# Optimization experiments

Hardware: AMD Instinct MI355X
Metric: run time of the kernel (lower is better)

## Reference

```python
import jax, jax.numpy as jnp
import numpy as np

L = 2        # lags
D = 8        # latent_size
H = 64       # hidden_dim
IN = L * D + 1
SLOPE = 0.2  # nn.LeakyReLU(0.2) as in the LEAP/TDRL NLayerLeakyMLP


def setup_inputs() -> dict:
    key = jax.random.key(0)
    ks = jax.random.split(key, 6)
    B, T = 128, 514
    def w(k, shape, fan_in):
        return jax.random.normal(k, shape, jnp.float32) * (1.0 / np.sqrt(fan_in))
    return {
        'x':  jax.random.normal(ks[0], (B, T, D), jnp.float32),
        # per-latent-dim stacked MLP params (D independent small MLPs)
        'W0': w(ks[1], (D, H, IN), IN), 'b0': jnp.zeros((D, H), jnp.float32),
        'W1': w(ks[2], (D, H, H), H),   'b1': jnp.zeros((D, H), jnp.float32),
        'W2': w(ks[3], (D, H, H), H),   'b2': jnp.zeros((D, H), jnp.float32),
        'Wo': w(ks[4], (D, 1, H), H),   'bo': jnp.zeros((D, 1), jnp.float32),
    }


def reference(x, W0, b0, W1, b1, W2, b2, Wo, bo):
    B, T, Dd = x.shape
    W = T - L                                   # number of windows
    N = B * W
    idx = jnp.arange(W)[:, None] + jnp.arange(L + 1)[None, :]
    xw = x[:, idx]                              # [B, W, L+1, D]
    yy = xw[:, :, :L].reshape(N, L * Dd)        # lagged history  [N, L*D]
    xx = xw[:, :, L].reshape(N, Dd)             # current step    [N, D]
    # per-dim inputs: concat(yy, xx[:, i])  -> [D, N, IN]
    inp = jnp.concatenate(
        [jnp.broadcast_to(yy[None], (Dd, N, L * Dd)), xx.T[:, :, None]], axis=-1)

    def lin(a, Wm, bm):  # batched over latent dim d
        return jnp.einsum('dni,dhi->dnh', a, Wm) + bm[:, None, :]

    h0 = lin(inp, W0, b0); m0 = jnp.where(h0 > 0, 1.0, SLOPE); a0 = h0 * m0
    h1 = lin(a0, W1, b1);  m1 = jnp.where(h1 > 0, 1.0, SLOPE); a1 = h1 * m1
    h2 = lin(a1, W2, b2);  m2 = jnp.where(h2 > 0, 1.0, SLOPE); a2 = h2 * m2
    out = jnp.einsum('dnh,doh->dno', a2, Wo) + bo[:, None, :]   # [D, N, 1]

    # analytic Jacobian of scalar output wrt input: Wo diag(m2) W2 diag(m1) W1 diag(m0) W0
    g = jnp.broadcast_to(Wo[:, 0][:, None, :], (Dd, N, H)) * m2
    g = jnp.einsum('dnh,dhg->dng', g, W2) * m1
    g = jnp.einsum('dnh,dhg->dng', g, W1) * m0
    jac = jnp.einsum('dnh,dhi->dni', g, W0)                     # [D, N, IN]

    residuals = out[:, :, 0].T.reshape(B, W, Dd)                # [B, W, D]
    logabsdet = jnp.sum(jnp.log(jnp.abs(jac[:, :, -1])), axis=0)  # sum over dims -> [N]
    sum_log_abs_det_jacobian = logabsdet.reshape(B, W).sum(axis=1)  # [B]
    hist_jac = jac[:, :, :-1]                                   # [D, N, L*D] (stacked list)
    return residuals, sum_log_abs_det_jacobian, hist_jac
```

## Files before the change

### kernel.cpp

```cpp
#include <hip/hip_runtime.h>
#include <hip/hip_bf16.h>
#include <math.h>

#define D_ 8
#define H_ 64
#define IN_ 17
#define SLOPE_ 0.2f
#define B_ 128
#define T_ 514
#define W_ 512
#define N_ (B_*W_)
#define RES_SZ (N_*D_)
#define LOG_OFF RES_SZ
#define HJ_OFF (RES_SZ + B_)

#define BSTR 72

#define PERD_B 23040
#define OB_W2H 0
#define OB_W2L 4608
#define OB_W1H 9216
#define OB_W1L 13824
#define OB_W0H 18432
#define OB_W0L 20736
#define FWD_U (D_*PERD_B)
#define PERD_F 27648
#define OF_W0H 0
#define OF_W0L 4608
#define OF_W1H 9216
#define OF_W1L 13824
#define OF_W2H 18432
#define OF_W2L 23040

typedef __attribute__((ext_vector_type(8))) short short8;
typedef __attribute__((ext_vector_type(4))) float float4v;

__device__ __forceinline__ unsigned short f2bf(float x) {
    return __bfloat16_as_ushort(__float2bfloat16(x));
}
__device__ __forceinline__ float bf2f(unsigned short h) {
    return __uint_as_float(((unsigned)h) << 16);
}
__device__ __forceinline__ void split2(float x, short& hi, short& lo) {
    unsigned short h = f2bf(x);
    hi = (short)h;
    float r = x - bf2f(h);
    lo = (short)f2bf(r);
}

__global__ void setup_kernel(const float* __restrict__ W0, const float* __restrict__ W1,
                             const float* __restrict__ W2,
                             unsigned short* __restrict__ ws, float* __restrict__ out) {
    int d = blockIdx.x;
    unsigned short* bb = ws + d * PERD_B;
    unsigned short* bf = ws + FWD_U + d * PERD_F;
    for (int idx = threadIdx.x; idx < H_ * H_; idx += blockDim.x) {
        int r = idx >> 6, c = idx & 63;
        float v2 = W2[d * H_ * H_ + c * H_ + r];
        unsigned short h2 = f2bf(v2);
        bb[OB_W2H + r * BSTR + c] = h2;
        bb[OB_W2L + r * BSTR + c] = f2bf(v2 - bf2f(h2));
        float v1 = W1[d * H_ * H_ + c * H_ + r];
        unsigned short h1 = f2bf(v1);
        bb[OB_W1H + r * BSTR + c] = h1;
        bb[OB_W1L + r * BSTR + c] = f2bf(v1 - bf2f(h1));
        float f1v = W1[(d * H_ + r) * H_ + c];
        unsigned short f1h = f2bf(f1v);
        bf[OF_W1H + r * BSTR + c] = f1h;
        bf[OF_W1L + r * BSTR + c] = f2bf(f1v - bf2f(f1h));
        float f2v = W2[(d * H_ + r) * H_ + c];
        unsigned short f2h = f2bf(f2v);
        bf[OF_W2H + r * BSTR + c] = f2h;
        bf[OF_W2L + r * BSTR + c] = f2bf(f2v - bf2f(f2h));
    }
    for (int idx = threadIdx.x; idx < 32 * H_; idx += blockDim.x) {
        int nn = idx >> 6, k = idx & 63;
        float v = (nn < IN_) ? W0[(d * H_ + k) * IN_ + nn] : 0.0f;
        unsigned short h = f2bf(v);
        bb[OB_W0H + nn * BSTR + k] = h;
        bb[OB_W0L + nn * BSTR + k] = f2bf(v - bf2f(h));
        float fv = (nn < IN_) ? W0[(d * H_ + k) * IN_ + nn] : 0.0f;
        unsigned short fh = f2bf(fv);
        bf[OF_W0H + k * BSTR + nn] = fh;
        bf[OF_W0L + k * BSTR + nn] = f2bf(fv - bf2f(fh));
    }
    if (d == 0 && threadIdx.x < B_) out[LOG_OFF + threadIdx.x] = 0.0f;
}

__global__ __launch_bounds__(256, 2) void fwdm_kernel(
    const float* __restrict__ x,
    const float* __restrict__ b0, const float* __restrict__ b1,
    const float* __restrict__ b2, const float* __restrict__ Wo,
    const float* __restrict__ bo, const unsigned short* __restrict__ ws,
    float* __restrict__ out)
{
    __shared__ __align__(16) unsigned short sB[PERD_F];
    __shared__ __align__(16) float sAct[4 * 16 * 68];
    __shared__ unsigned sM0[256*2], sM1[256*2], sM2[256*2];
    __shared__ __align__(16) float sWo[H_];

    const int blk = blockIdx.x;
    const int d   = blk >> 8;
    const int t   = blk & 255;
    const int tid = threadIdx.x;
    const int n0  = t << 8;

    {
        const uint4* src = (const uint4*)(ws + FWD_U + d * PERD_F);
        uint4* dst = (uint4*)sB;
        for (int i = tid; i < PERD_F / 8; i += 256) dst[i] = src[i];
        if (tid < H_) sWo[tid] = Wo[d * H_ + tid];
    }

    const int wv   = tid >> 6;
    const int lane = tid & 63;
    const int q    = lane >> 4;
    const int c    = lane & 15;
    float* slot = sAct + wv * (16 * 68);

    float b0v[4], b1v[4], b2v[4];
#pragma unroll
    for (int nt = 0; nt < 4; ++nt) {
        b0v[nt] = b0[d * H_ + nt * 16 + c];
        b1v[nt] = b1[d * H_ + nt * 16 + c];
        b2v[nt] = b2[d * H_ + nt * 16 + c];
    }
    const float bod = bo[d];
    __syncthreads();

#pragma unroll 1
    for (int mti = 0; mti < 4; ++mti) {
        const int sbase = wv * 64 + mti * 16;
        const int gn    = n0 + sbase + c;

        short8 ah[2], al[2];
        float4v acc[4];

        {
            const float* xp = x + (((gn >> 9) * T_) + (gn & 511)) * D_;
            float xs[8] = {0,0,0,0,0,0,0,0};
            if (q < 2) {
                float4 f0 = *(const float4*)(xp + q * 8);
                float4 f1 = *(const float4*)(xp + q * 8 + 4);
                xs[0]=f0.x; xs[1]=f0.y; xs[2]=f0.z; xs[3]=f0.w;
                xs[4]=f1.x; xs[5]=f1.y; xs[6]=f1.z; xs[7]=f1.w;
            } else if (q == 2) {
                xs[0] = xp[16 + d];
            }
#pragma unroll
            for (int j = 0; j < 8; ++j) { short h8,l8; split2(xs[j],h8,l8); ah[0][j]=h8; al[0][j]=l8; }
        }
#pragma unroll
        for (int nt = 0; nt < 4; ++nt) {
            int off = (nt*16 + c) * BSTR + (q << 3);
            short8 bh = *(const short8*)(sB + OF_W0H + off);
            short8 bl = *(const short8*)(sB + OF_W0L + off);
            float4v a = {0.f,0.f,0.f,0.f};
            a = __builtin_amdgcn_mfma_f32_16x16x32_bf16(ah[0], bh, a, 0,0,0);
            a = __builtin_amdgcn_mfma_f32_16x16x32_bf16(al[0], bh, a, 0,0,0);
            a = __builtin_amdgcn_mfma_f32_16x16x32_bf16(ah[0], bl, a, 0,0,0);
            acc[nt] = a;
        }
#pragma unroll
        for (int r = 0; r < 4; ++r) {
            float hv[4]; bool p[4];
#pragma unroll
            for (int nt = 0; nt < 4; ++nt) { hv[nt] = acc[nt][r] + b0v[nt]; p[nt] = hv[nt] > 0.0f; }
            unsigned long long B0 = __ballot(p[0]), B1 = __ballot(p[1]);
            unsigned long long B2 = __ballot(p[2]), B3 = __ballot(p[3]);
            if (c == 0) {
                int row = sbase + q * 4 + r;
                sM0[row*2]   = (unsigned)((B0 >> (q*16)) & 0xffffull) | ((unsigned)((B1 >> (q*16)) & 0xffffull) << 16);
                sM0[row*2+1] = (unsigned)((B2 >> (q*16)) & 0xffffull) | ((unsigned)((B3 >> (q*16)) & 0xffffull) << 16);
            }
#pragma unroll
            for (int nt = 0; nt < 4; ++nt)
                slot[(q*4+r)*68 + nt*16 + c] = p[nt] ? hv[nt] : hv[nt] * SLOPE_;
        }

#pragma unroll
        for (int kst = 0; kst < 2; ++kst) {
            const float* p = slot + c * 68 + kst * 32 + q * 8;
            float4 f0 = *(const float4*)p, f1 = *(const float4*)(p + 4);
            float xs[8] = {f0.x,f0.y,f0.z,f0.w,f1.x,f1.y,f1.z,f1.w};
#pragma unroll
            for (int j = 0; j < 8; ++j) { short h8,l8; split2(xs[j],h8,l8); ah[kst][j]=h8; al[kst][j]=l8; }
        }
#pragma unroll
        for (int nt = 0; nt < 4; ++nt) {
            float4v a = {0.f,0.f,0.f,0.f};
#pragma unroll
            for (int kst = 0; kst < 2; ++kst) {
                int off = (nt*16 + c) * BSTR + (kst << 5) + (q << 3);
                short8 bh = *(const short8*)(sB + OF_W1H + off);
                short8 bl = *(const short8*)(sB + OF_W1L + off);
                a = __builtin_amdgcn_mfma_f32_16x16x32_bf16(ah[kst], bh, a, 0,0,0);
                a = __builtin_amdgcn_mfma_f32_16x16x32_bf16(al[kst], bh, a, 0,0,0);
                a = __builtin_amdgcn_mfma_f32_16x16x32_bf16(ah[kst], bl, a, 0,0,0);
            }
            acc[nt] = a;
        }
#pragma unroll
        for (int r = 0; r < 4; ++r) {
            float hv[4]; bool p[4];
#pragma unroll
            for (int nt = 0; nt < 4; ++nt) { hv[nt] = acc[nt][r] + b1v[nt]; p[nt] = hv[nt] > 0.0f; }
            unsigned long long B0 = __ballot(p[0]), B1 = __ballot(p[1]);
            unsigned long long B2 = __ballot(p[2]), B3 = __ballot(p[3]);
            if (c == 0) {
                int row = sbase + q * 4 + r;
                sM1[row*2]   = (unsigned)((B0 >> (q*16)) & 0xffffull) | ((unsigned)((B1 >> (q*16)) & 0xffffull) << 16);
                sM1[row*2+1] = (unsigned)((B2 >> (q*16)) & 0xffffull) | ((unsigned)((B3 >> (q*16)) & 0xffffull) << 16);
            }
#pragma unroll
            for (int nt = 0; nt < 4; ++nt)
                slot[(q*4+r)*68 + nt*16 + c] = p[nt] ? hv[nt] : hv[nt] * SLOPE_;
        }

#pragma unroll
        for (int kst = 0; kst < 2; ++kst) {
            const float* p = slot + c * 68 + kst * 32 + q * 8;
            float4 f0 = *(const float4*)p, f1 = *(const float4*)(p + 4);
            float xs[8] = {f0.x,f0.y,f0.z,f0.w,f1.x,f1.y,f1.z,f1.w};
#pragma unroll
            for (int j = 0; j < 8; ++j) { short h8,l8; split2(xs[j],h8,l8); ah[kst][j]=h8; al[kst][j]=l8; }
        }
#pragma unroll
        for (int nt = 0; nt < 4; ++nt) {
            float4v a = {0.f,0.f,0.f,0.f};
#pragma unroll
            for (int kst = 0; kst < 2; ++kst) {
                int off = (nt*16 + c) * BSTR + (kst << 5) + (q << 3);
                short8 bh = *(const short8*)(sB + OF_W2H + off);
                short8 bl = *(const short8*)(sB + OF_W2L + off);
                a = __builtin_amdgcn_mfma_f32_16x16x32_bf16(ah[kst], bh, a, 0,0,0);
                a = __builtin_amdgcn_mfma_f32_16x16x32_bf16(al[kst], bh, a, 0,0,0);
                a = __builtin_amdgcn_mfma_f32_16x16x32_bf16(ah[kst], bl, a, 0,0,0);
            }
            acc[nt] = a;
        }
#pragma unroll
        for (int r = 0; r < 4; ++r) {
            float hv[4]; bool p[4];
#pragma unroll
            for (int nt = 0; nt < 4; ++nt) { hv[nt] = acc[nt][r] + b2v[nt]; p[nt] = hv[nt] > 0.0f; }
            unsigned long long B0 = __ballot(p[0]), B1 = __ballot(p[1]);
            unsigned long long B2 = __ballot(p[2]), B3 = __ballot(p[3]);
            if (c == 0) {
                int row = sbase + q * 4 + r;
                sM2[row*2]   = (unsigned)((B0 >> (q*16)) & 0xffffull) | ((unsigned)((B1 >> (q*16)) & 0xffffull) << 16);
                sM2[row*2+1] = (unsigned)((B2 >> (q*16)) & 0xffffull) | ((unsigned)((B3 >> (q*16)) & 0xffffull) << 16);
            }
#pragma unroll
            for (int nt = 0; nt < 4; ++nt)
                slot[(q*4+r)*68 + nt*16 + c] = p[nt] ? hv[nt] : hv[nt] * SLOPE_;
        }

        {
            const float* srow = slot + c * 68 + q * 16;
            const float* wop  = sWo + q * 16;
            float4 s0 = *(const float4*)srow,       s1 = *(const float4*)(srow + 4);
            float4 s2 = *(const float4*)(srow + 8), s3 = *(const float4*)(srow + 12);
            float4 w0 = *(const float4*)wop,        w1 = *(const float4*)(wop + 4);
            float4 w2 = *(const float4*)(wop + 8),  w3 = *(const float4*)(wop + 12);
            float part = s0.x*w0.x + s0.y*w0.y + s0.z*w0.z + s0.w*w0.w
                       + s1.x*w1.x + s1.y*w1.y + s1.z*w1.z + s1.w*w1.w
                       + s2.x*w2.x + s2.y*w2.y + s2.z*w2.z + s2.w*w2.w
                       + s3.x*w3.x + s3.y*w3.y + s3.z*w3.z + s3.w*w3.w;
            part += __shfl_xor(part, 16, 64);
            part += __shfl_xor(part, 32, 64);
            if (q == 0) out[gn * D_ + d] = part + bod;
        }
    }

    __syncthreads();
    {
        unsigned* outU = (unsigned*)out;
        size_t mi = (size_t)HJ_OFF + ((size_t)d * N_ + (n0 + tid)) * 16;
        outU[mi+0] = sM0[tid*2]; outU[mi+1] = sM0[tid*2+1];
        outU[mi+2] = sM1[tid*2]; outU[mi+3] = sM1[tid*2+1];
        outU[mi+4] = sM2[tid*2]; outU[mi+5] = sM2[tid*2+1];
    }
}

__global__ __launch_bounds__(256, 2) void bwd_kernel(
    const float* __restrict__ Wo,
    const unsigned short* __restrict__ ws,
    float* __restrict__ out)
{
    __shared__ __align__(16) unsigned short sB[PERD_B];
    __shared__ __align__(16) float sAct[4 * 16 * 68];
    __shared__ unsigned sM0[256*2], sM1[256*2], sM2[256*2];
    __shared__ float sWo[H_];
    __shared__ float sRed[4];

    const int blk = blockIdx.x;
    const int d   = blk >> 8;
    const int t   = blk & 255;
    const int tid = threadIdx.x;
    const int n0  = t << 8;

    {
        const uint4* src = (const uint4*)(ws + d * PERD_B);
        uint4* dst = (uint4*)sB;
        for (int i = tid; i < PERD_B / 8; i += 256) dst[i] = src[i];
        if (tid < H_) sWo[tid] = Wo[d * H_ + tid];
        const unsigned* outU = (const unsigned*)out;
        size_t mi = (size_t)HJ_OFF + ((size_t)d * N_ + (n0 + tid)) * 16;
        sM0[tid*2] = outU[mi+0]; sM0[tid*2+1] = outU[mi+1];
        sM1[tid*2] = outU[mi+2]; sM1[tid*2+1] = outU[mi+3];
        sM2[tid*2] = outU[mi+4]; sM2[tid*2+1] = outU[mi+5];
    }
    __syncthreads();

    const int wv   = tid >> 6;
    const int lane = tid & 63;
    const int q    = lane >> 4;
    const int c    = lane & 15;
    float* slot = sAct + wv * (16 * 68);

    short8 Bw2h[4][2], Bw2l[4][2], Bw1h[4][2], Bw1l[4][2], Bw0h[2][2], Bw0l[2][2];
#pragma unroll
    for (int nt = 0; nt < 4; ++nt)
#pragma unroll
        for (int kst = 0; kst < 2; ++kst) {
            int off = (nt*16 + c) * BSTR + (kst << 5) + (q << 3);
            Bw2h[nt][kst] = *(const short8*)(sB + OB_W2H + off);
            Bw2l[nt][kst] = *(const short8*)(sB + OB_W2L + off);
            Bw1h[nt][kst] = *(const short8*)(sB + OB_W1H + off);
            Bw1l[nt][kst] = *(const short8*)(sB + OB_W1L + off);
        }
#pragma unroll
    for (int nt = 0; nt < 2; ++nt)
#pragma unroll
        for (int kst = 0; kst < 2; ++kst) {
            int off = (nt*16 + c) * BSTR + (kst << 5) + (q << 3);
            Bw0h[nt][kst] = *(const short8*)(sB + OB_W0H + off);
            Bw0l[nt][kst] = *(const short8*)(sB + OB_W0L + off);
        }

    float ld = 0.0f;

#pragma unroll 1
    for (int mti = 0; mti < 4; ++mti) {
        const int sbase = wv * 64 + mti * 16;

        short8 ah[2];
        float4v acc[4];

#pragma unroll
        for (int kst = 0; kst < 2; ++kst) {
            unsigned mm = sM2[(sbase + c) * 2 + kst];
            const float* wop = sWo + kst * 32 + q * 8;
            float4 e0 = *(const float4*)wop, e1 = *(const float4*)(wop + 4);
            float xs[8] = {e0.x,e0.y,e0.z,e0.w,e1.x,e1.y,e1.z,e1.w};
#pragma unroll
            for (int j = 0; j < 8; ++j) {
                int kk = q * 8 + j;
                float v = xs[j] * (((mm >> kk) & 1u) ? 1.0f : SLOPE_);
                ah[kst][j] = (short)f2bf(v);
            }
        }
#pragma unroll
        for (int nt = 0; nt < 4; ++nt) {
            float4v a = {0.f,0.f,0.f,0.f};
#pragma unroll
            for (int kst = 0; kst < 2; ++kst) {
                a = __builtin_amdgcn_mfma_f32_16x16x32_bf16(ah[kst], Bw2h[nt][kst], a, 0,0,0);
                a = __builtin_amdgcn_mfma_f32_16x16x32_bf16(ah[kst], Bw2l[nt][kst], a, 0,0,0);
            }
            acc[nt] = a;
        }
#pragma unroll
        for (int nt = 0; nt < 4; ++nt)
#pragma unroll
            for (int r = 0; r < 4; ++r) {
                int row = q * 4 + r, col = nt * 16 + c;
                unsigned bit = (sM1[(sbase + row) * 2 + (col >> 5)] >> (col & 31)) & 1u;
                float v = acc[nt][r];
                slot[row * 68 + col] = bit ? v : v * SLOPE_;
            }

#pragma unroll
        for (int kst = 0; kst < 2; ++kst) {
            const float* p = slot + c * 68 + kst * 32 + q * 8;
            float4 f0 = *(const float4*)p, f1 = *(const float4*)(p + 4);
            float xs[8] = {f0.x,f0.y,f0.z,f0.w,f1.x,f1.y,f1.z,f1.w};
#pragma unroll
            for (int j = 0; j < 8; ++j) ah[kst][j] = (short)f2bf(xs[j]);
        }
#pragma unroll
        for (int nt = 0; nt < 4; ++nt) {
            float4v a = {0.f,0.f,0.f,0.f};
#pragma unroll
            for (int kst = 0; kst < 2; ++kst) {
                a = __builtin_amdgcn_mfma_f32_16x16x32_bf16(ah[kst], Bw1h[nt][kst], a, 0,0,0);
                a = __builtin_amdgcn_mfma_f32_16x16x32_bf16(ah[kst], Bw1l[nt][kst], a, 0,0,0);
            }
            acc[nt] = a;
        }
#pragma unroll
        for (int nt = 0; nt < 4; ++nt)
#pragma unroll
            for (int r = 0; r < 4; ++r) {
                int row = q * 4 + r, col = nt * 16 + c;
                unsigned bit = (sM0[(sbase + row) * 2 + (col >> 5)] >> (col & 31)) & 1u;
                float v = acc[nt][r];
                slot[row * 68 + col] = bit ? v : v * SLOPE_;
            }

#pragma unroll
        for (int kst = 0; kst < 2; ++kst) {
            const float* p = slot + c * 68 + kst * 32 + q * 8;
            float4 f0 = *(const float4*)p, f1 = *(const float4*)(p + 4);
            float xs[8] = {f0.x,f0.y,f0.z,f0.w,f1.x,f1.y,f1.z,f1.w};
#pragma unroll
            for (int j = 0; j < 8; ++j) ah[kst][j] = (short)f2bf(xs[j]);
        }
#pragma unroll
        for (int nt = 0; nt < 2; ++nt) {
            float4v a = {0.f,0.f,0.f,0.f};
#pragma unroll
            for (int kst = 0; kst < 2; ++kst) {
                a = __builtin_amdgcn_mfma_f32_16x16x32_bf16(ah[kst], Bw0h[nt][kst], a, 0,0,0);
                a = __builtin_amdgcn_mfma_f32_16x16x32_bf16(ah[kst], Bw0l[nt][kst], a, 0,0,0);
            }
            acc[nt] = a;
        }
#pragma unroll
        for (int r = 0; r < 4; ++r) {
            int gn = n0 + sbase + q * 4 + r;
            out[HJ_OFF + ((size_t)d * N_ + gn) * 16 + c] = acc[0][r];
        }
        if (c == 0) {
#pragma unroll
            for (int r = 0; r < 4; ++r) ld += logf(fabsf(acc[1][r]));
        }
    }

#pragma unroll
    for (int off = 32; off > 0; off >>= 1)
        ld += __shfl_down(ld, off, 64);
    if (lane == 0) sRed[wv] = ld;
    __syncthreads();
    if (tid == 0)
        atomicAdd(out + LOG_OFF + (t >> 1), (sRed[0] + sRed[1]) + (sRed[2] + sRed[3]));
}

extern "C" void kernel_launch(void* const* d_in, const int* in_sizes, int n_in,
                              void* d_out, int out_size, void* d_ws, size_t ws_size,
                              hipStream_t stream) {
    const float* x  = (const float*)d_in[0];
    const float* W0 = (const float*)d_in[1];
    const float* b0 = (const float*)d_in[2];
    const float* W1 = (const float*)d_in[3];
    const float* b1 = (const float*)d_in[4];
    const float* W2 = (const float*)d_in[5];
    const float* b2 = (const float*)d_in[6];
    const float* Wo = (const float*)d_in[7];
    const float* bo = (const float*)d_in[8];
    float* out = (float*)d_out;
    unsigned short* ws = (unsigned short*)d_ws;

    hipLaunchKernelGGL(setup_kernel, dim3(D_), dim3(256), 0, stream, W0, W1, W2, ws, out);
    hipLaunchKernelGGL(fwdm_kernel, dim3(D_ * 256), dim3(256), 0, stream,
                       x, b0, b1, b2, Wo, bo, ws, out);
    hipLaunchKernelGGL(bwd_kernel, dim3(D_ * 256), dim3(256), 0, stream,
                       Wo, ws, out);
}
```

Measured before the change: 217.5 us.

## Fuse forward and backward Jacobian kernels into a single launch

Merges the forward (activation and mask) kernel and the backward Jacobian kernel into one kernel. The leaky-ReLU masks stay in shared memory instead of being written to global memory and read back. The backward weight fragments are loaded straight from global workspace into registers rather than staged through shared memory. This drops one launch and the mask round trip through global memory, but keeping all the backward weight fragments in registers for the whole kernel raises register pressure and may hurt occupancy or cause spills.

```diff
diff --git a/kernel.cpp b/kernel.cpp
--- a/kernel.cpp
+++ b/kernel.cpp
@@ -87,7 +87,7 @@
     if (d == 0 && threadIdx.x < B_) out[LOG_OFF + threadIdx.x] = 0.0f;
 }
 
-__global__ __launch_bounds__(256, 2) void fwdm_kernel(
+__global__ __launch_bounds__(256, 2) void fused_kernel(
     const float* __restrict__ x,
     const float* __restrict__ b0, const float* __restrict__ b1,
     const float* __restrict__ b2, const float* __restrict__ Wo,
@@ -98,6 +98,7 @@
     __shared__ __align__(16) float sAct[4 * 16 * 68];
     __shared__ unsigned sM0[256*2], sM1[256*2], sM2[256*2];
     __shared__ __align__(16) float sWo[H_];
+    __shared__ float sRed[4];
 
     const int blk = blockIdx.x;
     const int d   = blk >> 8;
@@ -117,6 +118,27 @@
     const int q    = lane >> 4;
     const int c    = lane & 15;
     float* slot = sAct + wv * (16 * 68);
+
+    const unsigned short* wb = ws + (size_t)d * PERD_B;
+    short8 Bw2h[4][2], Bw2l[4][2], Bw1h[4][2], Bw1l[4][2], Bw0h[2][2], Bw0l[2][2];
+#pragma unroll
+    for (int nt = 0; nt < 4; ++nt)
+#pragma unroll
+        for (int kst = 0; kst < 2; ++kst) {
+            int off = (nt*16 + c) * BSTR + (kst << 5) + (q << 3);
+            Bw2h[nt][kst] = *(const short8*)(wb + OB_W2H + off);
+            Bw2l[nt][kst] = *(const short8*)(wb + OB_W2L + off);
+            Bw1h[nt][kst] = *(const short8*)(wb + OB_W1H + off);
+            Bw1l[nt][kst] = *(const short8*)(wb + OB_W1L + off);
+        }
+#pragma unroll
+    for (int nt = 0; nt < 2; ++nt)
+#pragma unroll
+        for (int kst = 0; kst < 2; ++kst) {
+            int off = (nt*16 + c) * BSTR + (kst << 5) + (q << 3);
+            Bw0h[nt][kst] = *(const short8*)(wb + OB_W0H + off);
+            Bw0l[nt][kst] = *(const short8*)(wb + OB_W0L + off);
+        }
 
     float b0v[4], b1v[4], b2v[4];
 #pragma unroll
@@ -273,72 +295,6 @@
         }
     }
 
-    __syncthreads();
-    {
-        unsigned* outU = (unsigned*)out;
-        size_t mi = (size_t)HJ_OFF + ((size_t)d * N_ + (n0 + tid)) * 16;
-        outU[mi+0] = sM0[tid*2]; outU[mi+1] = sM0[tid*2+1];
-        outU[mi+2] = sM1[tid*2]; outU[mi+3] = sM1[tid*2+1];
-        outU[mi+4] = sM2[tid*2]; outU[mi+5] = sM2[tid*2+1];
-    }
-}
-
-__global__ __launch_bounds__(256, 2) void bwd_kernel(
-    const float* __restrict__ Wo,
-    const unsigned short* __restrict__ ws,
-    float* __restrict__ out)
-{
-    __shared__ __align__(16) unsigned short sB[PERD_B];
-    __shared__ __align__(16) float sAct[4 * 16 * 68];
-    __shared__ unsigned sM0[256*2], sM1[256*2], sM2[256*2];
-    __shared__ float sWo[H_];
-    __shared__ float sRed[4];
-
-    const int blk = blockIdx.x;
-    const int d   = blk >> 8;
-    const int t   = blk & 255;
-    const int tid = threadIdx.x;
-    const int n0  = t << 8;
-
-    {
-        const uint4* src = (const uint4*)(ws + d * PERD_B);
-        uint4* dst = (uint4*)sB;
-        for (int i = tid; i < PERD_B / 8; i += 256) dst[i] = src[i];
-        if (tid < H_) sWo[tid] = Wo[d * H_ + tid];
-        const unsigned* outU = (const unsigned*)out;
-        size_t mi = (size_t)HJ_OFF + ((size_t)d * N_ + (n0 + tid)) * 16;
-        sM0[tid*2] = outU[mi+0]; sM0[tid*2+1] = outU[mi+1];
-        sM1[tid*2] = outU[mi+2]; sM1[tid*2+1] = outU[mi+3];
-        sM2[tid*2] = outU[mi+4]; sM2[tid*2+1] = outU[mi+5];
-    }
-    __syncthreads();
-
-    const int wv   = tid >> 6;
-    const int lane = tid & 63;
-    const int q    = lane >> 4;
-    const int c    = lane & 15;
-    float* slot = sAct + wv * (16 * 68);
-
-    short8 Bw2h[4][2], Bw2l[4][2], Bw1h[4][2], Bw1l[4][2], Bw0h[2][2], Bw0l[2][2];
-#pragma unroll
-    for (int nt = 0; nt < 4; ++nt)
-#pragma unroll
-        for (int kst = 0; kst < 2; ++kst) {
-            int off = (nt*16 + c) * BSTR + (kst << 5) + (q << 3);
-            Bw2h[nt][kst] = *(const short8*)(sB + OB_W2H + off);
-            Bw2l[nt][kst] = *(const short8*)(sB + OB_W2L + off);
-            Bw1h[nt][kst] = *(const short8*)(sB + OB_W1H + off);
-            Bw1l[nt][kst] = *(const short8*)(sB + OB_W1L + off);
-        }
-#pragma unroll
-    for (int nt = 0; nt < 2; ++nt)
-#pragma unroll
-        for (int kst = 0; kst < 2; ++kst) {
-            int off = (nt*16 + c) * BSTR + (kst << 5) + (q << 3);
-            Bw0h[nt][kst] = *(const short8*)(sB + OB_W0H + off);
-            Bw0l[nt][kst] = *(const short8*)(sB + OB_W0L + off);
-        }
-
     float ld = 0.0f;
 
 #pragma unroll 1
@@ -463,8 +419,6 @@
     unsigned short* ws = (unsigned short*)d_ws;
 
     hipLaunchKernelGGL(setup_kernel, dim3(D_), dim3(256), 0, stream, W0, W1, W2, ws, out);
-    hipLaunchKernelGGL(fwdm_kernel, dim3(D_ * 256), dim3(256), 0, stream,
+    hipLaunchKernelGGL(fused_kernel, dim3(D_ * 256), dim3(256), 0, stream,
                        x, b0, b1, b2, Wo, bo, ws, out);
-    hipLaunchKernelGGL(bwd_kernel, dim3(D_ * 256), dim3(256), 0, stream,
-                       Wo, ws, out);
-}
+}
```

Result: faster. 198.9 us (-8.6%).
